# Optimization experiments

Hardware: AMD Instinct MI355X
Metric: run time of the kernel (lower is better)

## Reference

```python
import jax, jax.numpy as jnp
import numpy as np

# H2RConfig constants
KERNEL = 3
MAX_ROUTES = 1000
STRIDE = 4.0
MIN_SIZE = 32.0
MAX_SIZE = 512.0
SCORE_POWER = 2.0
UNC_WEIGHT = 0.35


def setup_inputs() -> dict:
    key = jax.random.key(0)
    k1, k2, k3 = jax.random.split(key, 3)
    shape = (32, 1, 512, 512)  # [B, 1, H, W] heatmaps at stride 4
    return {
        "route_logits": jax.random.normal(k1, shape, jnp.float32),
        "scale_logits": jax.random.normal(k2, shape, jnp.float32),
        "uncertainty_logits": jax.random.normal(k3, shape, jnp.float32),
        "image_h": 2048,
        "image_w": 2048,
    }


def reference(route_logits, scale_logits, uncertainty_logits, image_h, image_w):
    # score map: sigmoid^power, modulated by uncertainty (use_route_uncertainty=True)
    score = jnp.power(jax.nn.sigmoid(route_logits), SCORE_POWER)
    score = score * (1.0 - UNC_WEIGHT * jax.nn.sigmoid(uncertainty_logits))

    # local-max NMS: 3x3 max pool, stride 1, SAME padding (torch pads with -inf)
    pooled = jax.lax.reduce_window(
        score, -jnp.inf, jax.lax.max,
        window_dimensions=(1, 1, KERNEL, KERNEL),
        window_strides=(1, 1, 1, 1),
        padding="SAME",
    )
    peak_mask = score == pooled
    filtered = jnp.where(peak_mask, score, -1.0)

    B = score.shape[0]
    Wd = score.shape[3]
    flat = filtered.reshape(B, -1)                 # [B, H*W]
    values, indices = jax.lax.top_k(flat, MAX_ROUTES)  # [B, K]
    valid = values > 0.0                            # torch drops these; we mask/pad

    ys = indices // Wd
    xs = indices % Wd
    cx = (xs.astype(jnp.float32) + 0.5) * STRIDE
    cy = (ys.astype(jnp.float32) + 0.5) * STRIDE

    # gather scale / uncertainty at peak locations
    sc = jnp.take_along_axis(scale_logits.reshape(B, -1), indices, axis=1)
    un = jax.nn.sigmoid(jnp.take_along_axis(uncertainty_logits.reshape(B, -1), indices, axis=1))

    side = MIN_SIZE + jax.nn.sigmoid(sc) * (MAX_SIZE - MIN_SIZE)
    side = side * (1.0 + 0.25 * un)
    half = side * 0.5

    iw = float(image_w)
    ih = float(image_h)
    x1 = jnp.clip(cx - half, 0.0, iw - 1.0)
    y1 = jnp.clip(cy - half, 0.0, ih - 1.0)
    x2 = jnp.clip(cx + half, 1.0, iw)
    y2 = jnp.clip(cy + half, 1.0, ih)

    bcol = jnp.broadcast_to(jnp.arange(B, dtype=jnp.float32)[:, None], values.shape)
    rois = jnp.stack([bcol, x1, y1, x2, y2], axis=-1)  # [B, K, 5]

    # padded (fixed-shape) equivalent of torch's variable-length concat
    rois = jnp.where(valid[..., None], rois, 0.0)
    scores = jnp.where(valid, values, 0.0)
    return rois, scores, valid
```

## Files before the change

kernel.cpp:

```cpp
#include <hip/hip_runtime.h>
#include <hip/hip_bf16.h>
#include <math.h>


#define B_   32
#define H_   512
#define W_   512
#define HW_  (H_ * W_)
#define K_   1000
#define ROWS_ 16
#define THR_  512
#define NSTRIP_ 32
#define WSEGCAP_ 176
#define STRIPCAP_ (8 * WSEGCAP_)
#define NSLOT_ (NSTRIP_ * STRIPCAP_)
#define NPAIR_ (NSLOT_ / 2)
#define CAND_ 2048
#define NBUK_ 4096
#define GSPLIT_ 8
#define SPLITCAP_ 512

#define PL_BYTES_ ((size_t)B_ * NSLOT_ * 8)
#define GH_BYTES_ ((size_t)B_ * NBUK_ * 4)
#define GC_BYTES_ ((size_t)B_ * GSPLIT_ * 4)
#define CD_BYTES_ ((size_t)B_ * GSPLIT_ * SPLITCAP_ * 8)

__device__ __forceinline__ float np_expf(float x) {
#pragma clang fp contract(off)
    const float log2e = 1.44269504088896341f;
    float z = x * log2e;
    float m = rintf(z);
    float r = fmaf(m, -0.693359375f, x);
    r = fmaf(m, 2.12194440e-4f, r);
    float r2 = r * r;
    float p = fmaf(1.9875691500e-4f, r, 1.3981999507e-3f);
    p = fmaf(p, r, 8.3334519073e-3f);
    p = fmaf(p, r, 4.1665795894e-2f);
    p = fmaf(p, r, 1.6666665459e-1f);
    p = fmaf(p, r, 5.0000001201e-1f);
    p = fmaf(p, r2, r);
    p = p + 1.0f;
    int mi = (int)m;
    float sc = __int_as_float((127 + mi) << 23);
    return p * sc;
}

__device__ __forceinline__ float sigmoid_np(float x) {
#pragma clang fp contract(off)
    float e = np_expf(-x);
    float d = 1.0f + e;
    return 1.0f / d;
}

__device__ __forceinline__ float score_ref(float r, float u) {
#pragma clang fp contract(off)
    float s  = sigmoid_np(r);
    float s2 = s * s;
    float su = sigmoid_np(u);
    float t  = 0.35f * su;
    float m  = 1.0f - t;
    return s2 * m;
}

__device__ __forceinline__ float sigmoid_fast(float x) {
    return 1.0f / (1.0f + __expf(-x));
}

__global__ __launch_bounds__(THR_, 4) void fused_peak_kernel(
    const float* __restrict__ route, const float* __restrict__ unc,
    unsigned long long* __restrict__ plist,
    unsigned int* __restrict__ ghist)
{
    __shared__ float sm[ROWS_ + 2][W_];

    const int tid   = threadIdx.x;
    const int lane  = tid & 63;
    const int wid   = tid >> 6;
    const int strip = blockIdx.x;
    const int b     = blockIdx.y;
    const int r0    = strip * ROWS_;

    const float4* rb4 = (const float4*)(route + (size_t)b * HW_);
    const float4* ub4 = (const float4*)(unc   + (size_t)b * HW_);
    unsigned long long* wseg =
        plist + (size_t)(b * NSTRIP_ + strip) * STRIPCAP_ + wid * WSEGCAP_;

    float4 rv[5], uv[5];
    int lrow[5], c4[5]; bool ok[5];
    #pragma unroll
    for (int k = 0; k < 5; ++k) {
        int slot = tid + k * THR_;
        slot = slot < 2303 ? slot : 2303;
        int row = slot >> 7;
        int gy  = r0 - 1 + row;
        lrow[k] = row; c4[k] = slot & 127;
        ok[k]   = (gy >= 0 && gy < H_);
        int cy  = gy < 0 ? 0 : (gy >= H_ ? H_ - 1 : gy);
        rv[k] = rb4[cy * 128 + c4[k]];
        uv[k] = ub4[cy * 128 + c4[k]];
    }
    #pragma unroll
    for (int k = 0; k < 5; ++k) {
        float4 s;
        s.x = score_ref(rv[k].x, uv[k].x);
        s.y = score_ref(rv[k].y, uv[k].y);
        s.z = score_ref(rv[k].z, uv[k].z);
        s.w = score_ref(rv[k].w, uv[k].w);
        if (!ok[k]) { s.x = -INFINITY; s.y = -INFINITY;
                      s.z = -INFINITY; s.w = -INFINITY; }
        *(float4*)&sm[lrow[k]][c4[k] * 4] = s;
    }
    __syncthreads();

    const unsigned long long lt = (1ull << lane) - 1ull;
    int wn = 0;
    unsigned int hreg[8];
    #pragma unroll
    for (int j = 0; j < 4; ++j) {
        int g  = tid + j * THR_;
        int ly = 1 + (g >> 7);
        int x0 = (g & 127) * 4;
        int gy = r0 + (ly - 1);
        float4 q0 = *(const float4*)&sm[ly - 1][x0];
        float4 q1 = *(const float4*)&sm[ly    ][x0];
        float4 q2 = *(const float4*)&sm[ly + 1][x0];
        bool hasL = (x0 > 0), hasR = (x0 + 4 < W_);
        float l0 = hasL ? sm[ly - 1][x0 - 1] : -INFINITY;
        float l1 = hasL ? sm[ly    ][x0 - 1] : -INFINITY;
        float l2 = hasL ? sm[ly + 1][x0 - 1] : -INFINITY;
        float e0 = hasR ? sm[ly - 1][x0 + 4] : -INFINITY;
        float e1 = hasR ? sm[ly    ][x0 + 4] : -INFINITY;
        float e2 = hasR ? sm[ly + 1][x0 + 4] : -INFINITY;
        float f_m1 = fmaxf(l0, fmaxf(l1, l2));
        float f_0  = fmaxf(q0.x, fmaxf(q1.x, q2.x));
        float f_1  = fmaxf(q0.y, fmaxf(q1.y, q2.y));
        float f_2  = fmaxf(q0.z, fmaxf(q1.z, q2.z));
        float f_3  = fmaxf(q0.w, fmaxf(q1.w, q2.w));
        float f_4  = fmaxf(e0, fmaxf(e1, e2));
        float tb0  = fmaxf(q0.x, q2.x);
        float tb1  = fmaxf(q0.y, q2.y);
        float tb2  = fmaxf(q0.z, q2.z);
        float tb3  = fmaxf(q0.w, q2.w);
        float vv[4] = { q1.x, q1.y, q1.z, q1.w };
        float mm[4];
        mm[0] = fmaxf(fmaxf(f_m1, f_1), tb0);
        mm[1] = fmaxf(fmaxf(f_0,  f_2), tb1);
        mm[2] = fmaxf(fmaxf(f_1,  f_3), tb2);
        mm[3] = fmaxf(fmaxf(f_2,  f_4), tb3);
        unsigned int pk01 = 0u, pk23 = 0u;
        #pragma unroll
        for (int i = 0; i < 4; ++i) {
            bool take = (vv[i] >= mm[i]);
            unsigned long long mk = __ballot(take);
            if (take) {
                int p = wn + __popcll(mk & lt);
                if (p < WSEGCAP_) {
                    unsigned int bits = __float_as_uint(vv[i]);
                    unsigned int idx  = (unsigned int)(gy * W_ + x0 + i);
                    wseg[p] = ((unsigned long long)bits << 32)
                              | (0xFFFFFFFFu - idx);
                    unsigned int bkt = bits >> 18;
                    if (i < 2) pk01 |= bkt << (16 * i);
                    else       pk23 |= bkt << (16 * (i - 2));
                }
            }
            wn += __popcll(mk);
        }
        hreg[2 * j]     = pk01;
        hreg[2 * j + 1] = pk23;
    }
    for (int i = (wn < WSEGCAP_ ? wn : WSEGCAP_) + lane; i < WSEGCAP_; i += 64)
        wseg[i] = 0ull;
    __syncthreads();

    unsigned int* hist = (unsigned int*)&sm[0][0];
    for (int i = tid; i < NBUK_; i += THR_) hist[i] = 0u;
    __syncthreads();

    #pragma unroll
    for (int j = 0; j < 8; ++j) {
        unsigned int h  = hreg[j];
        unsigned int b0 = h & 0xFFFFu;
        unsigned int b1 = h >> 16;
        if (b0) atomicAdd(&hist[b0], 1u);
        if (b1) atomicAdd(&hist[b1], 1u);
    }
    __syncthreads();

    unsigned int* gh = ghist + (size_t)b * NBUK_;
    for (int i = tid; i < NBUK_; i += THR_) {
        unsigned int c = hist[i];
        if (c) atomicAdd(&gh[i], c);
    }
}

__global__ __launch_bounds__(1024) void gather_kernel(
    const unsigned long long* __restrict__ plist,
    const unsigned int* __restrict__ ghist,
    int* __restrict__ gcnt8,
    unsigned long long* __restrict__ gcand)
{
    __shared__ int sh_T, sh_n;

    const int sp  = blockIdx.x;
    const int b   = blockIdx.y;
    const int tid = threadIdx.x;
    const int lane = tid & 63, wid = tid >> 6;

    const ulonglong2* p2 = (const ulonglong2*)(plist + (size_t)b * NSLOT_);
    const int i0 = sp * (NPAIR_ / GSPLIT_);
    const int i1 = i0 + (NPAIR_ / GSPLIT_);

    ulonglong2 a[3]; int ni = 0;
    {
        int k = 0;
        for (int i = i0 + tid; i < i1; i += 1024, ++k) a[k] = p2[i];
        ni = k;
    }

    if (tid == 0) { sh_T = 0; sh_n = 0; }
    if (wid == 0) {
        const unsigned int* gh = ghist + (size_t)b * NBUK_;
        int total = 0;
        for (int c = NBUK_ / 64 - 1; c >= 0; --c) {
            int cnt = (int)gh[c * 64 + lane];
            int sum = cnt;
            #pragma unroll
            for (int off = 32; off > 0; off >>= 1)
                sum += __shfl_down(sum, off, 64);
            sum = __shfl(sum, 0, 64);
            if (total + sum < K_) { total += sum; continue; }
            int suf = cnt;
            #pragma unroll
            for (int off = 1; off < 64; off <<= 1) {
                int o = __shfl_down(suf, off, 64);
                suf += (lane + off < 64) ? o : 0;
            }
            bool cond = (total + suf) >= K_;
            unsigned long long mask = __ballot(cond);
            int ls = 63 - __builtin_clzll(mask);
            if (lane == 0) sh_T = c * 64 + ls;
            break;
        }
    }
    __syncthreads();
    unsigned int T = (unsigned int)sh_T;
    if (T == 0u) T = 1u;

    unsigned long long* cd =
        gcand + ((size_t)b * GSPLIT_ + sp) * SPLITCAP_;
    for (int k = 0; k < ni; ++k) {
        unsigned long long ks[2] = { a[k].x, a[k].y };
        #pragma unroll
        for (int q = 0; q < 2; ++q) {
            bool take = ((((unsigned int)(ks[q] >> 32))) >> 18) >= T;
            unsigned long long mk = __ballot(take);
            if (mk) {
                int ldr = __ffsll((unsigned long long)mk) - 1;
                int base_ = 0;
                if (lane == ldr) base_ = atomicAdd(&sh_n, __popcll(mk));
                base_ = __shfl(base_, ldr, 64);
                if (take) {
                    int p = base_ + __popcll(mk & ((1ull << lane) - 1ull));
                    if (p < SPLITCAP_) cd[p] = ks[q];
                }
            }
        }
    }
    __syncthreads();
    if (tid == 0) {
        int n = sh_n; if (n > SPLITCAP_) n = SPLITCAP_;
        gcnt8[b * GSPLIT_ + sp] = n;
    }
}

__global__ __launch_bounds__(1024) void sort_emit_kernel(
    const float* __restrict__ scale, const float* __restrict__ unc,
    const unsigned long long* __restrict__ gcand,
    const int* __restrict__ gcnt8,
    const int* __restrict__ ih_p, const int* __restrict__ iw_p,
    float* __restrict__ out)
{
    __shared__ unsigned long long cand[CAND_];
    __shared__ int offs[GSPLIT_ + 1];

    const int b = blockIdx.x, tid = threadIdx.x;
    if (tid == 0) {
        int r = 0;
        #pragma unroll
        for (int s = 0; s < GSPLIT_; ++s) {
            offs[s] = r;
            r += gcnt8[b * GSPLIT_ + s];
        }
        offs[GSPLIT_] = r;
    }
    __syncthreads();
    int nc = offs[GSPLIT_]; if (nc > CAND_) nc = CAND_;
    int sortN = (nc <= 1024) ? 1024 : CAND_;

    const unsigned long long* cd = gcand + (size_t)b * GSPLIT_ * SPLITCAP_;
    for (int i = tid; i < GSPLIT_ * SPLITCAP_; i += 1024) {
        int s = i >> 9;
        int k = i & (SPLITCAP_ - 1);
        int c0 = offs[s];
        if (k < offs[s + 1] - c0) {
            int d = c0 + k;
            if (d < CAND_) cand[d] = cd[i];
        }
    }
    for (int i = tid; i < sortN; i += 1024)
        if (i >= nc) cand[i] = 0ull;

    for (int kk = 2; kk <= sortN; kk <<= 1) {
        for (int jj = kk >> 1; jj > 0; jj >>= 1) {
            __syncthreads();
            for (int p = tid; p < (sortN >> 1); p += 1024) {
                int i   = ((p & ~(jj - 1)) << 1) | (p & (jj - 1));
                int ixj = i | jj;
                bool desc = ((i & kk) == 0);
                unsigned long long a = cand[i], c2 = cand[ixj];
                if (desc ? (a < c2) : (a > c2)) { cand[i] = c2; cand[ixj] = a; }
            }
        }
    }
    __syncthreads();

    const float fih = (float)(*ih_p);
    const float fiw = (float)(*iw_p);
    float* rois   = out;
    float* scores = out + (size_t)B_ * K_ * 5;
    float* validf = out + (size_t)B_ * K_ * 6;

    for (int k = tid; k < K_; k += 1024) {
        int o = b * K_ + k;
        unsigned long long key = cand[k];
        unsigned int bits = (unsigned int)(key >> 32);
        if (bits == 0u) {
            rois[o * 5 + 0] = 0.0f; rois[o * 5 + 1] = 0.0f;
            rois[o * 5 + 2] = 0.0f; rois[o * 5 + 3] = 0.0f;
            rois[o * 5 + 4] = 0.0f;
            scores[o] = 0.0f; validf[o] = 0.0f;
        } else {
            float v = __uint_as_float(bits);
            unsigned int idx = 0xFFFFFFFFu - (unsigned int)(key & 0xFFFFFFFFull);
            int y = (int)(idx >> 9), x = (int)(idx & 511u);
            float cx = ((float)x + 0.5f) * 4.0f;
            float cy = ((float)y + 0.5f) * 4.0f;
            float ss = sigmoid_fast(scale[(size_t)b * HW_ + idx]);
            float su = sigmoid_fast(unc  [(size_t)b * HW_ + idx]);
            float side = (32.0f + ss * 480.0f) * (1.0f + 0.25f * su);
            float half = 0.5f * side;
            float x1 = fminf(fmaxf(cx - half, 0.0f), fiw - 1.0f);
            float y1 = fminf(fmaxf(cy - half, 0.0f), fih - 1.0f);
            float x2 = fminf(fmaxf(cx + half, 1.0f), fiw);
            float y2 = fminf(fmaxf(cy + half, 1.0f), fih);
            rois[o * 5 + 0] = (float)b;
            rois[o * 5 + 1] = x1; rois[o * 5 + 2] = y1;
            rois[o * 5 + 3] = x2; rois[o * 5 + 4] = y2;
            scores[o] = v; validf[o] = 1.0f;
        }
    }
}

extern "C" void kernel_launch(void* const* d_in, const int* in_sizes, int n_in,
                              void* d_out, int out_size, void* d_ws, size_t ws_size,
                              hipStream_t stream) {
    const float* route = (const float*)d_in[0];
    const float* scale = (const float*)d_in[1];
    const float* unc   = (const float*)d_in[2];
    const int*   ih    = (const int*)d_in[3];
    const int*   iw    = (const int*)d_in[4];
    float* out = (float*)d_out;

    unsigned char* base = (unsigned char*)d_ws;
    unsigned long long* plist = (unsigned long long*)base;
    unsigned int* ghist = (unsigned int*)(base + PL_BYTES_);
    int* gcnt8          = (int*)(base + PL_BYTES_ + GH_BYTES_);
    unsigned long long* gcand =
        (unsigned long long*)(base + PL_BYTES_ + GH_BYTES_ + GC_BYTES_);

    hipMemsetAsync(ghist, 0, GH_BYTES_, stream);

    dim3 g(NSTRIP_, B_);
    fused_peak_kernel<<<g, THR_, 0, stream>>>(route, unc, plist, ghist);
    dim3 gg(GSPLIT_, B_);
    gather_kernel<<<gg, 1024, 0, stream>>>(plist, ghist, gcnt8, gcand);
    sort_emit_kernel<<<B_, 1024, 0, stream>>>(scale, unc, gcand, gcnt8,
                                              ih, iw, out);
}
```

Before: 185.0 us.

## Replace gather and bitonic sort with bucket-scatter rank selection in one kernel

The peak kernel now writes per-strip packed 16-bit histograms directly, instead of global atomics into a memset buffer. A single per-batch select kernel sums these histograms and finds the threshold bucket. It prefix-sums bucket cursors, scatters candidates into bucket-ordered shared memory, and ranks each candidate by counting larger keys within its bucket. This removes the memset, one kernel launch, and the multi-pass bitonic sort. In exchange, only 32 blocks now scan the whole peak list for each batch, and a crowded bucket can make within-bucket ranking quadratic.

After: 164.5 us. -11.1%, faster.

```diff
diff --git a/kernel.cpp b/kernel.cpp
--- a/kernel.cpp
+++ b/kernel.cpp
@@ -15,15 +15,12 @@
 #define STRIPCAP_ (8 * WSEGCAP_)
 #define NSLOT_ (NSTRIP_ * STRIPCAP_)
 #define NPAIR_ (NSLOT_ / 2)
-#define CAND_ 2048
 #define NBUK_ 4096
-#define GSPLIT_ 8
-#define SPLITCAP_ 512
-
-#define PL_BYTES_ ((size_t)B_ * NSLOT_ * 8)
-#define GH_BYTES_ ((size_t)B_ * NBUK_ * 4)
-#define GC_BYTES_ ((size_t)B_ * GSPLIT_ * 4)
-#define CD_BYTES_ ((size_t)B_ * GSPLIT_ * SPLITCAP_ * 8)
+#define NW2_  (NBUK_ / 2)
+#define GCAP_ 2048
+
+#define PL_BYTES_  ((size_t)B_ * NSLOT_ * 8)
+#define GH2_BYTES_ ((size_t)B_ * NSTRIP_ * NW2_ * 4)
 
 __device__ __forceinline__ float np_expf(float x) {
 #pragma clang fp contract(off)
@@ -69,7 +66,7 @@
 __global__ __launch_bounds__(THR_, 4) void fused_peak_kernel(
     const float* __restrict__ route, const float* __restrict__ unc,
     unsigned long long* __restrict__ plist,
-    unsigned int* __restrict__ ghist)
+    unsigned int* __restrict__ ghist2)
 {
     __shared__ float sm[ROWS_ + 2][W_];
 
@@ -174,7 +171,7 @@
     __syncthreads();
 
     unsigned int* hist = (unsigned int*)&sm[0][0];
-    for (int i = tid; i < NBUK_; i += THR_) hist[i] = 0u;
+    for (int i = tid; i < NW2_; i += THR_) hist[i] = 0u;
     __syncthreads();
 
     #pragma unroll
@@ -182,48 +179,49 @@
         unsigned int h  = hreg[j];
         unsigned int b0 = h & 0xFFFFu;
         unsigned int b1 = h >> 16;
-        if (b0) atomicAdd(&hist[b0], 1u);
-        if (b1) atomicAdd(&hist[b1], 1u);
-    }
-    __syncthreads();
-
-    unsigned int* gh = ghist + (size_t)b * NBUK_;
-    for (int i = tid; i < NBUK_; i += THR_) {
-        unsigned int c = hist[i];
-        if (c) atomicAdd(&gh[i], c);
-    }
-}
-
-__global__ __launch_bounds__(1024) void gather_kernel(
+        if (b0) atomicAdd(&hist[b0 >> 1], 1u << ((b0 & 1) * 16));
+        if (b1) atomicAdd(&hist[b1 >> 1], 1u << ((b1 & 1) * 16));
+    }
+    __syncthreads();
+
+    unsigned int* gh2 = ghist2 + (size_t)(b * NSTRIP_ + strip) * NW2_;
+    for (int i = tid; i < NW2_; i += THR_) gh2[i] = hist[i];
+}
+
+__global__ __launch_bounds__(1024) void select2_kernel(
+    const float* __restrict__ scale, const float* __restrict__ unc,
     const unsigned long long* __restrict__ plist,
-    const unsigned int* __restrict__ ghist,
-    int* __restrict__ gcnt8,
-    unsigned long long* __restrict__ gcand)
+    const unsigned int* __restrict__ ghist2,
+    const int* __restrict__ ih_p, const int* __restrict__ iw_p,
+    float* __restrict__ out)
 {
-    __shared__ int sh_T, sh_n;
-
-    const int sp  = blockIdx.x;
-    const int b   = blockIdx.y;
-    const int tid = threadIdx.x;
+    __shared__ unsigned int hist[NBUK_];
+    __shared__ unsigned int cursor[NBUK_];
+    __shared__ unsigned long long grp[GCAP_];
+    __shared__ int sh_T, sh_nc;
+
+    const int b = blockIdx.x, tid = threadIdx.x;
     const int lane = tid & 63, wid = tid >> 6;
 
-    const ulonglong2* p2 = (const ulonglong2*)(plist + (size_t)b * NSLOT_);
-    const int i0 = sp * (NPAIR_ / GSPLIT_);
-    const int i1 = i0 + (NPAIR_ / GSPLIT_);
-
-    ulonglong2 a[3]; int ni = 0;
-    {
-        int k = 0;
-        for (int i = i0 + tid; i < i1; i += 1024, ++k) a[k] = p2[i];
-        ni = k;
-    }
-
-    if (tid == 0) { sh_T = 0; sh_n = 0; }
+    const unsigned int* gbase = ghist2 + (size_t)b * NSTRIP_ * NW2_;
+    for (int w = tid; w < NW2_; w += 1024) {
+        unsigned int s0 = 0u, s1 = 0u;
+        #pragma unroll
+        for (int s = 0; s < NSTRIP_; ++s) {
+            unsigned int v = gbase[s * NW2_ + w];
+            s0 += v & 0xFFFFu;
+            s1 += v >> 16;
+        }
+        hist[2 * w]     = s0;
+        hist[2 * w + 1] = s1;
+    }
+    __syncthreads();
+
     if (wid == 0) {
-        const unsigned int* gh = ghist + (size_t)b * NBUK_;
+        int Tv = 0;
         int total = 0;
         for (int c = NBUK_ / 64 - 1; c >= 0; --c) {
-            int cnt = (int)gh[c * 64 + lane];
+            int cnt = (int)hist[c * 64 + lane];
             int sum = cnt;
             #pragma unroll
             for (int off = 32; off > 0; off >>= 1)
@@ -239,87 +237,43 @@
             bool cond = (total + suf) >= K_;
             unsigned long long mask = __ballot(cond);
             int ls = 63 - __builtin_clzll(mask);
-            if (lane == 0) sh_T = c * 64 + ls;
+            Tv = c * 64 + ls;
             break;
         }
-    }
-    __syncthreads();
-    unsigned int T = (unsigned int)sh_T;
-    if (T == 0u) T = 1u;
-
-    unsigned long long* cd =
-        gcand + ((size_t)b * GSPLIT_ + sp) * SPLITCAP_;
-    for (int k = 0; k < ni; ++k) {
-        unsigned long long ks[2] = { a[k].x, a[k].y };
-        #pragma unroll
-        for (int q = 0; q < 2; ++q) {
-            bool take = ((((unsigned int)(ks[q] >> 32))) >> 18) >= T;
-            unsigned long long mk = __ballot(take);
-            if (mk) {
-                int ldr = __ffsll((unsigned long long)mk) - 1;
-                int base_ = 0;
-                if (lane == ldr) base_ = atomicAdd(&sh_n, __popcll(mk));
-                base_ = __shfl(base_, ldr, 64);
-                if (take) {
-                    int p = base_ + __popcll(mk & ((1ull << lane) - 1ull));
-                    if (p < SPLITCAP_) cd[p] = ks[q];
-                }
-            }
-        }
-    }
-    __syncthreads();
-    if (tid == 0) {
-        int n = sh_n; if (n > SPLITCAP_) n = SPLITCAP_;
-        gcnt8[b * GSPLIT_ + sp] = n;
-    }
-}
-
-__global__ __launch_bounds__(1024) void sort_emit_kernel(
-    const float* __restrict__ scale, const float* __restrict__ unc,
-    const unsigned long long* __restrict__ gcand,
-    const int* __restrict__ gcnt8,
-    const int* __restrict__ ih_p, const int* __restrict__ iw_p,
-    float* __restrict__ out)
-{
-    __shared__ unsigned long long cand[CAND_];
-    __shared__ int offs[GSPLIT_ + 1];
-
-    const int b = blockIdx.x, tid = threadIdx.x;
-    if (tid == 0) {
-        int r = 0;
-        #pragma unroll
-        for (int s = 0; s < GSPLIT_; ++s) {
-            offs[s] = r;
-            r += gcnt8[b * GSPLIT_ + s];
-        }
-        offs[GSPLIT_] = r;
-    }
-    __syncthreads();
-    int nc = offs[GSPLIT_]; if (nc > CAND_) nc = CAND_;
-    int sortN = (nc <= 1024) ? 1024 : CAND_;
-
-    const unsigned long long* cd = gcand + (size_t)b * GSPLIT_ * SPLITCAP_;
-    for (int i = tid; i < GSPLIT_ * SPLITCAP_; i += 1024) {
-        int s = i >> 9;
-        int k = i & (SPLITCAP_ - 1);
-        int c0 = offs[s];
-        if (k < offs[s + 1] - c0) {
-            int d = c0 + k;
-            if (d < CAND_) cand[d] = cd[i];
-        }
-    }
-    for (int i = tid; i < sortN; i += 1024)
-        if (i >= nc) cand[i] = 0ull;
-
-    for (int kk = 2; kk <= sortN; kk <<= 1) {
-        for (int jj = kk >> 1; jj > 0; jj >>= 1) {
-            __syncthreads();
-            for (int p = tid; p < (sortN >> 1); p += 1024) {
-                int i   = ((p & ~(jj - 1)) << 1) | (p & (jj - 1));
-                int ixj = i | jj;
-                bool desc = ((i & kk) == 0);
-                unsigned long long a = cand[i], c2 = cand[ixj];
-                if (desc ? (a < c2) : (a > c2)) { cand[i] = c2; cand[ixj] = a; }
+        if (Tv < 1) Tv = 1;
+
+        int run = 0;
+        for (int cb = NBUK_ - 64; cb >= (Tv & ~63); cb -= 64) {
+            int beta = cb + lane;
+            int cnt = (beta >= Tv) ? (int)hist[beta] : 0;
+            int suf = cnt;
+            #pragma unroll
+            for (int off = 1; off < 64; off <<= 1) {
+                int o = __shfl_down(suf, off, 64);
+                suf += (lane + off < 64) ? o : 0;
+            }
+            int chunk_total = __shfl(suf, 0, 64);
+            if (beta >= Tv) cursor[beta] = (unsigned int)(run + (suf - cnt));
+            run += chunk_total;
+        }
+        if (lane == 0) { sh_T = Tv; sh_nc = run; }
+    }
+    __syncthreads();
+    const unsigned int T = (unsigned int)sh_T;
+
+    {
+        const ulonglong2* p2 = (const ulonglong2*)(plist + (size_t)b * NSLOT_);
+        for (int i = tid; i < NPAIR_; i += 1024) {
+            ulonglong2 a = p2[i];
+            unsigned int b0 = (unsigned int)(a.x >> 50);
+            unsigned int b1 = (unsigned int)(a.y >> 50);
+            if (b0 >= T) {
+                unsigned int pos = atomicAdd(&cursor[b0], 1u);
+                if (pos < GCAP_) grp[pos] = a.x;
+            }
+            if (b1 >= T) {
+                unsigned int pos = atomicAdd(&cursor[b1], 1u);
+                if (pos < GCAP_) grp[pos] = a.y;
             }
         }
     }
@@ -331,16 +285,21 @@
     float* scores = out + (size_t)B_ * K_ * 5;
     float* validf = out + (size_t)B_ * K_ * 6;
 
-    for (int k = tid; k < K_; k += 1024) {
-        int o = b * K_ + k;
-        unsigned long long key = cand[k];
-        unsigned int bits = (unsigned int)(key >> 32);
-        if (bits == 0u) {
-            rois[o * 5 + 0] = 0.0f; rois[o * 5 + 1] = 0.0f;
-            rois[o * 5 + 2] = 0.0f; rois[o * 5 + 3] = 0.0f;
-            rois[o * 5 + 4] = 0.0f;
-            scores[o] = 0.0f; validf[o] = 0.0f;
-        } else {
+    int nc = sh_nc;
+    int ncEff = nc < GCAP_ ? nc : GCAP_;
+    for (int p = tid; p < ncEff; p += 1024) {
+        unsigned long long key = grp[p];
+        unsigned int beta = (unsigned int)(key >> 50);
+        int segEnd   = (int)cursor[beta];
+        int segStart = segEnd - (int)hist[beta];
+        int qEnd = segEnd < GCAP_ ? segEnd : GCAP_;
+        int r = 0;
+        for (int q = segStart; q < qEnd; ++q)
+            r += (grp[q] > key) ? 1 : 0;
+        int rank = segStart + r;
+        if (rank < K_) {
+            int o = b * K_ + rank;
+            unsigned int bits = (unsigned int)(key >> 32);
             float v = __uint_as_float(bits);
             unsigned int idx = 0xFFFFFFFFu - (unsigned int)(key & 0xFFFFFFFFull);
             int y = (int)(idx >> 9), x = (int)(idx & 511u);
@@ -360,6 +319,13 @@
             scores[o] = v; validf[o] = 1.0f;
         }
     }
+    for (int k = nc + tid; k < K_; k += 1024) {
+        int o = b * K_ + k;
+        rois[o * 5 + 0] = 0.0f; rois[o * 5 + 1] = 0.0f;
+        rois[o * 5 + 2] = 0.0f; rois[o * 5 + 3] = 0.0f;
+        rois[o * 5 + 4] = 0.0f;
+        scores[o] = 0.0f; validf[o] = 0.0f;
+    }
 }
 
 extern "C" void kernel_launch(void* const* d_in, const int* in_sizes, int n_in,
@@ -374,17 +340,10 @@
 
     unsigned char* base = (unsigned char*)d_ws;
     unsigned long long* plist = (unsigned long long*)base;
-    unsigned int* ghist = (unsigned int*)(base + PL_BYTES_);
-    int* gcnt8          = (int*)(base + PL_BYTES_ + GH_BYTES_);
-    unsigned long long* gcand =
-        (unsigned long long*)(base + PL_BYTES_ + GH_BYTES_ + GC_BYTES_);
-
-    hipMemsetAsync(ghist, 0, GH_BYTES_, stream);
+    unsigned int* ghist2 = (unsigned int*)(base + PL_BYTES_);
 
     dim3 g(NSTRIP_, B_);
-    fused_peak_kernel<<<g, THR_, 0, stream>>>(route, unc, plist, ghist);
-    dim3 gg(GSPLIT_, B_);
-    gather_kernel<<<gg, 1024, 0, stream>>>(plist, ghist, gcnt8, gcand);
-    sort_emit_kernel<<<B_, 1024, 0, stream>>>(scale, unc, gcand, gcnt8,
-                                              ih, iw, out);
-}
+    fused_peak_kernel<<<g, THR_, 0, stream>>>(route, unc, plist, ghist2);
+    select2_kernel<<<B_, 1024, 0, stream>>>(scale, unc, plist, ghist2,
+                                            ih, iw, out);
+}
```
